# Performance work log

Measured on AMD Instinct MI355X. Metric: run time of the kernel, lower is better.

Reference implementation:

```python
import jax, jax.numpy as jnp
import numpy as np

HEAD_DIM = 256
L2_EPS = 1e-12  # tf.math.l2_normalize default epsilon


def setup_inputs() -> dict:
    key = jax.random.key(0)
    ks = jax.random.split(key, 6)
    B, U = 64, 2048
    D_dec, D_enc = 1024, 512
    H, K, A = 4, HEAD_DIM, 1024
    s = 0.075  # RandomUniform(-0.075, 0.075) kernel init
    return {
        "dec_state": jax.random.normal(ks[0], (B, D_dec), jnp.float32),
        "enc_state": jax.random.normal(ks[1], (B, U, D_enc), jnp.float32),
        "phi_w": jax.random.uniform(ks[2], (H, D_dec, K), jnp.float32, -s, s),
        "phi_b": jnp.zeros((H, K), jnp.float32),
        "psi_w": jax.random.uniform(ks[3], (H, D_enc, K), jnp.float32, -s, s),
        "psi_b": jnp.zeros((H, K), jnp.float32),
        "out_w": jax.random.uniform(ks[4], (H * D_enc, A), jnp.float32, -s, s),
        "out_b": jnp.zeros((A,), jnp.float32),
    }


def reference(dec_state, enc_state, phi_w, phi_b, psi_w, psi_b, out_w, out_b):
    B = dec_state.shape[0]
    # Per-head query/key projections, all heads at once.
    phi_s = jnp.einsum("bd,hdk->bhk", dec_state, phi_w) + phi_b[None]      # (B,H,K)
    psi_h = jnp.einsum("bue,hek->bhuk", enc_state, psi_w) + psi_b[None, :, None]  # (B,H,U,K)
    scale = 1.0 / jnp.sqrt(jnp.asarray(HEAD_DIM, jnp.float32))
    energy = jnp.einsum("bhk,bhuk->bhu", phi_s, psi_h) * scale              # (B,H,U)
    attn = jax.nn.softmax(energy, axis=-1)
    # NOTE: the original attends over the RAW enc_state (not psi_h).
    ctx = jnp.einsum("bhu,bue->bhe", attn, enc_state)                        # (B,H,E)
    # tf.math.l2_normalize over last axis
    sq = jnp.sum(ctx * ctx, axis=-1, keepdims=True)
    ctx = ctx * jax.lax.rsqrt(jnp.maximum(sq, L2_EPS))
    combined = ctx.reshape(B, -1)                                            # (B, H*E) == concat over heads
    return combined @ out_w + out_b
```

## Files before the change

kernel.cpp:

```cpp
#include <hip/hip_runtime.h>
#include <math.h>

typedef float f2 __attribute__((ext_vector_type(2)));

constexpr int NB = 64;
constexpr int NU = 2048;
constexpr int ND = 1024;
constexpr int NE = 512;
constexpr int NH = 4;
constexpr int NK = 256;
constexpr int NA = 1024;
constexpr int NS = 16;
constexpr int ROWS_PER_BLOCK = NU / NS;
constexpr int ROWS_PER_WAVE  = ROWS_PER_BLOCK / 4;
constexpr float SCALE = 0.0625f;

constexpr int RSPLIT = 16;
constexpr int RCH = (NH*NE)/RSPLIT;
constexpr int BT = 8;

constexpr int DSP = 16;

constexpr size_t WS_Q   = 0;
constexpr size_t WS_CTX = WS_Q + (size_t)NB*NH*NE;
constexpr size_t WS_P   = WS_CTX + (size_t)NB*NH*NE;

__global__ __launch_bounds__(256) void k_phi(
    const float* __restrict__ dec, const float* __restrict__ phi_w,
    float* __restrict__ P, float* __restrict__ q, float* __restrict__ ctxacc,
    const float* __restrict__ out_b, float* __restrict__ out)
{
  const int flat = blockIdx.x;
  const int kc = flat & 3;
  const int h  = (flat >> 2) & 3;
  const int ds = flat >> 4;
  const int t = threadIdx.x;

  ctxacc[(size_t)flat*512 + t]       = 0.f;
  ctxacc[(size_t)flat*512 + 256 + t] = 0.f;
  q[(size_t)flat*512 + t]            = 0.f;
  q[(size_t)flat*512 + 256 + t]      = 0.f;
  out[(size_t)flat*256 + t] = out_b[(flat*256 + t) & (NA-1)];

  const int d0 = ds*64, k0 = kc*64;

  __shared__ float phi_lds[64][64];
  __shared__ float dec_t[64][68];

  {
    const int kq = t & 15, r = t >> 4;
    const float* pwb = phi_w + ((size_t)h*ND + d0)*NK + k0;
    #pragma unroll
    for (int p = 0; p < 4; ++p) {
      float4 v = *(const float4*)(pwb + (size_t)(r + 16*p)*NK + 4*kq);
      *(float4*)&phi_lds[r + 16*p][4*kq] = v;
    }
    const float* db = dec + d0 + 4*kq;
    #pragma unroll
    for (int p = 0; p < 4; ++p) {
      const int b = r + 16*p;
      float4 v = *(const float4*)(db + (size_t)b*ND);
      dec_t[4*kq+0][b] = v.x; dec_t[4*kq+1][b] = v.y;
      dec_t[4*kq+2][b] = v.z; dec_t[4*kq+3][b] = v.w;
    }
  }
  __syncthreads();

  const int k = t & 63, bq = t >> 6, b0 = bq*16;
  f2 acc2[8];
  #pragma unroll
  for (int i = 0; i < 8; ++i) acc2[i] = f2{0.f, 0.f};
  #pragma unroll 4
  for (int d = 0; d < 64; ++d) {
    float w = phi_lds[d][k];
    f2 ww = f2{w, w};
    float4 a0 = *(const float4*)&dec_t[d][b0];
    float4 a1 = *(const float4*)&dec_t[d][b0+4];
    float4 a2 = *(const float4*)&dec_t[d][b0+8];
    float4 a3 = *(const float4*)&dec_t[d][b0+12];
    acc2[0] += f2{a0.x,a0.y}*ww; acc2[1] += f2{a0.z,a0.w}*ww;
    acc2[2] += f2{a1.x,a1.y}*ww; acc2[3] += f2{a1.z,a1.w}*ww;
    acc2[4] += f2{a2.x,a2.y}*ww; acc2[5] += f2{a2.z,a2.w}*ww;
    acc2[6] += f2{a3.x,a3.y}*ww; acc2[7] += f2{a3.z,a3.w}*ww;
  }
  float* pb = P + (((size_t)ds*64 + b0)*NH + h)*NK + k0 + k;
  #pragma unroll
  for (int j = 0; j < 8; ++j) {
    pb[(size_t)(2*j  )*NH*NK] = acc2[j][0];
    pb[(size_t)(2*j+1)*NH*NK] = acc2[j][1];
  }
}

__global__ __launch_bounds__(256) void k_q(
    const float* __restrict__ P, const float* __restrict__ phi_b,
    const float* __restrict__ psi_w, float* __restrict__ q)
{
  const int flat = blockIdx.x;
  const int ks = flat & 3;
  const int ec = (flat >> 2) & 7;
  const int h  = flat >> 5;
  const int t = threadIdx.x;
  const int k0 = ks*64, e0 = ec*64;

  __shared__ float phi_red[64][68];
  __shared__ float psi_lds[64][65];

  {
    const int e = t >> 2, kq4 = t & 3;
    const float* pb = psi_w + ((size_t)h*NE + e0 + e)*NK + k0 + 4*kq4;
    #pragma unroll
    for (int p = 0; p < 4; ++p) {
      float4 v = *(const float4*)(pb + 16*p);
      const int kk = 4*(kq4 + 4*p);
      psi_lds[e][kk+0] = v.x; psi_lds[e][kk+1] = v.y;
      psi_lds[e][kk+2] = v.z; psi_lds[e][kk+3] = v.w;
    }
  }
  {
    const int b = t >> 2, kq4 = t & 3;
    const float* pbase = P + ((size_t)b*NH + h)*NK + k0 + 4*kq4;
    #pragma unroll
    for (int p = 0; p < 4; ++p) {
      float4 s = make_float4(0.f, 0.f, 0.f, 0.f);
      #pragma unroll
      for (int dsi = 0; dsi < DSP; ++dsi) {
        float4 v = *(const float4*)(pbase + (size_t)dsi*64*NH*NK + 16*p);
        s.x += v.x; s.y += v.y; s.z += v.z; s.w += v.w;
      }
      const int kk = 4*(kq4 + 4*p);
      const float* bb = phi_b + h*NK + k0 + kk;
      phi_red[kk+0][b] = s.x + bb[0];
      phi_red[kk+1][b] = s.y + bb[1];
      phi_red[kk+2][b] = s.z + bb[2];
      phi_red[kk+3][b] = s.w + bb[3];
    }
  }
  __syncthreads();

  const int e = t & 63, bq = t >> 6, b0 = bq*16;
  f2 acc2[8];
  #pragma unroll
  for (int i = 0; i < 8; ++i) acc2[i] = f2{0.f, 0.f};
  #pragma unroll 4
  for (int kl = 0; kl < 64; ++kl) {
    float w = psi_lds[e][kl];
    f2 ww = f2{w, w};
    float4 a0 = *(const float4*)&phi_red[kl][b0];
    float4 a1 = *(const float4*)&phi_red[kl][b0+4];
    float4 a2 = *(const float4*)&phi_red[kl][b0+8];
    float4 a3 = *(const float4*)&phi_red[kl][b0+12];
    acc2[0] += f2{a0.x,a0.y}*ww; acc2[1] += f2{a0.z,a0.w}*ww;
    acc2[2] += f2{a1.x,a1.y}*ww; acc2[3] += f2{a1.z,a1.w}*ww;
    acc2[4] += f2{a2.x,a2.y}*ww; acc2[5] += f2{a2.z,a2.w}*ww;
    acc2[6] += f2{a3.x,a3.y}*ww; acc2[7] += f2{a3.z,a3.w}*ww;
  }
  float* qb = q + ((size_t)b0*NH + h)*NE + e0 + e;
  #pragma unroll
  for (int j = 0; j < 8; ++j) {
    unsafeAtomicAdd(qb + (size_t)(2*j  )*NH*NE, acc2[j][0]);
    unsafeAtomicAdd(qb + (size_t)(2*j+1)*NH*NE, acc2[j][1]);
  }
}

__global__ __launch_bounds__(256, 4) void k_flash(
    const float* __restrict__ enc, const float* __restrict__ qg,
    float* __restrict__ ctxacc)
{
  const int s = blockIdx.x;
  const int b = blockIdx.y;
  const int t = threadIdx.x;
  const int wave = t >> 6;
  const int lane = t & 63;

  f2 qv[NH][4];
  const float* qb = qg + (size_t)b*NH*NE;
  #pragma unroll
  for (int h = 0; h < NH; ++h) {
    float4 a0 = *(const float4*)(qb + h*NE + 4*lane);
    float4 a1 = *(const float4*)(qb + h*NE + 256 + 4*lane);
    qv[h][0] = f2{a0.x, a0.y}; qv[h][1] = f2{a0.z, a0.w};
    qv[h][2] = f2{a1.x, a1.y}; qv[h][3] = f2{a1.z, a1.w};
  }
  f2 acc2[NH][4];
  #pragma unroll
  for (int h = 0; h < NH; ++h)
    #pragma unroll
    for (int j = 0; j < 4; ++j) acc2[h][j] = f2{0.f, 0.f};

  const int u0 = s*ROWS_PER_BLOCK + wave*ROWS_PER_WAVE;
  const float* encb = enc + ((size_t)b*NU + u0)*NE;
  #pragma unroll 2
  for (int r = 0; r < ROWS_PER_WAVE; ++r) {
    float4 v0 = *(const float4*)(encb + (size_t)r*NE + 4*lane);
    float4 v1 = *(const float4*)(encb + (size_t)r*NE + 256 + 4*lane);
    f2 e0 = f2{v0.x, v0.y}, e1 = f2{v0.z, v0.w};
    f2 e2 = f2{v1.x, v1.y}, e3 = f2{v1.z, v1.w};
    float d[NH];
    #pragma unroll
    for (int h = 0; h < NH; ++h) {
      f2 p = e0*qv[h][0] + e1*qv[h][1] + e2*qv[h][2] + e3*qv[h][3];
      d[h] = p[0] + p[1];
    }
    #pragma unroll
    for (int off = 1; off < 64; off <<= 1) {
      #pragma unroll
      for (int h = 0; h < NH; ++h) d[h] += __shfl_xor(d[h], off);
    }
    #pragma unroll
    for (int h = 0; h < NH; ++h) {
      float pf = __expf(d[h] * SCALE);
      f2 pp = f2{pf, pf};
      acc2[h][0] += pp*e0; acc2[h][1] += pp*e1;
      acc2[h][2] += pp*e2; acc2[h][3] += pp*e3;
    }
  }
  __shared__ float acc_lds[4][NH][NE];
  #pragma unroll
  for (int h = 0; h < NH; ++h) {
    *(float4*)&acc_lds[wave][h][4*lane] =
        make_float4(acc2[h][0][0], acc2[h][0][1], acc2[h][1][0], acc2[h][1][1]);
    *(float4*)&acc_lds[wave][h][256 + 4*lane] =
        make_float4(acc2[h][2][0], acc2[h][2][1], acc2[h][3][0], acc2[h][3][1]);
  }
  __syncthreads();
  float* cb = ctxacc + (size_t)b*(NH*NE);
  #pragma unroll
  for (int h = 0; h < NH; ++h) {
    #pragma unroll
    for (int eo = 0; eo < 2; ++eo) {
      int e = t + eo*256;
      float v = acc_lds[0][h][e] + acc_lds[1][h][e] + acc_lds[2][h][e] + acc_lds[3][h][e];
      unsafeAtomicAdd(&cb[h*NE + e], v);
    }
  }
}

__global__ __launch_bounds__(256) void k_out(
    const float* __restrict__ ctxacc, const float* __restrict__ out_w,
    float* __restrict__ out)
{
  const int t = threadIdx.x;
  const int a = blockIdx.x*256 + t;
  const int b0 = blockIdx.y * BT;
  const int rc = blockIdx.z;
  const int h  = rc >> 2;
  const int e0 = (rc & 3) * RCH;

  __shared__ float rn_lds[BT];
  const int wv = t >> 6, lane = t & 63;
  {
    const int i = 2*wv + (lane >> 5);
    const int l32 = lane & 31;
    const float* row = ctxacc + (size_t)(b0+i)*(NH*NE) + (size_t)h*NE;
    float ss = 0.f;
    #pragma unroll
    for (int j = 0; j < 16; ++j) { float v = row[l32 + 32*j]; ss += v*v; }
    #pragma unroll
    for (int off = 1; off < 32; off <<= 1) ss += __shfl_xor(ss, off);
    if (l32 == 0) rn_lds[i] = rsqrtf(fmaxf(ss, 1e-12f));
  }
  __syncthreads();

  __shared__ float c_lds[RCH][BT];
  for (int g = t; g < RCH*BT; g += 256) {
    const int r = g & (RCH-1), i = g >> 7;
    c_lds[r][i] = ctxacc[(size_t)(b0+i)*(NH*NE) + (size_t)h*NE + e0 + r] * rn_lds[i];
  }
  __syncthreads();

  float accv[BT];
  #pragma unroll
  for (int i = 0; i < BT; ++i) accv[i] = 0.f;
  const float* w = out_w + ((size_t)rc*RCH)*NA + a;
  #pragma unroll 8
  for (int r = 0; r < RCH; ++r) {
    float wvv = w[(size_t)r*NA];
    float4 ca = *(const float4*)&c_lds[r][0];
    float4 cb = *(const float4*)&c_lds[r][4];
    accv[0] += ca.x*wvv; accv[1] += ca.y*wvv; accv[2] += ca.z*wvv; accv[3] += ca.w*wvv;
    accv[4] += cb.x*wvv; accv[5] += cb.y*wvv; accv[6] += cb.z*wvv; accv[7] += cb.w*wvv;
  }
  #pragma unroll
  for (int i = 0; i < BT; ++i)
    unsafeAtomicAdd(&out[(size_t)(b0+i)*NA + a], accv[i]);
}

extern "C" void kernel_launch(void* const* d_in, const int* in_sizes, int n_in,
                              void* d_out, int out_size, void* d_ws, size_t ws_size,
                              hipStream_t stream) {
  const float* dec   = (const float*)d_in[0];
  const float* enc   = (const float*)d_in[1];
  const float* phi_w = (const float*)d_in[2];
  const float* phi_b = (const float*)d_in[3];
  const float* psi_w = (const float*)d_in[4];
  const float* out_w = (const float*)d_in[6];
  const float* out_b = (const float*)d_in[7];
  float* out = (float*)d_out;
  float* ws = (float*)d_ws;
  float* q      = ws + WS_Q;
  float* ctxacc = ws + WS_CTX;
  float* P      = ws + WS_P;

  hipLaunchKernelGGL(k_phi,   dim3(NH*4*DSP),              dim3(256), 0, stream,
                     dec, phi_w, P, q, ctxacc, out_b, out);
  hipLaunchKernelGGL(k_q,     dim3(128),                   dim3(256), 0, stream,
                     P, phi_b, psi_w, q);
  hipLaunchKernelGGL(k_flash, dim3(NS, NB),                dim3(256), 0, stream,
                     enc, q, ctxacc);
  hipLaunchKernelGGL(k_out,   dim3(NA/256, NB/BT, RSPLIT), dim3(256), 0, stream,
                     ctxacc, out_w, out);
}
```

Measured before the change: 84.71 us.

## Double-buffer encoder rows into LDS with async global_load_lds in flash kernel

The flash kernel now streams encoder rows through a per-wave double-buffered LDS staging area using direct global-to-LDS loads. It waits on vmcnt so the next two rows are in flight while the current two are processed, which is meant to hide global memory latency. It also folds the softmax scale into q up front, drops the occupancy hint in launch_bounds, and reuses the staging buffer for the final reduction. The risks are LDS round-trip overhead, reliance on manual waitcnt correctness, and possibly lower occupancy.

After: 91.18 us. +7.6%, slower.

```diff
diff --git a/kernel.cpp b/kernel.cpp
--- a/kernel.cpp
+++ b/kernel.cpp
@@ -162,7 +162,7 @@
   }
 }
 
-__global__ __launch_bounds__(256, 4) void k_flash(
+__global__ __launch_bounds__(256) void k_flash(
     const float* __restrict__ enc, const float* __restrict__ qg,
     float* __restrict__ ctxacc)
 {
@@ -172,14 +172,16 @@
   const int wave = t >> 6;
   const int lane = t & 63;
 
+  __shared__ float sbuf[4][2][2*NE];
+
   f2 qv[NH][4];
   const float* qb = qg + (size_t)b*NH*NE;
   #pragma unroll
   for (int h = 0; h < NH; ++h) {
     float4 a0 = *(const float4*)(qb + h*NE + 4*lane);
     float4 a1 = *(const float4*)(qb + h*NE + 256 + 4*lane);
-    qv[h][0] = f2{a0.x, a0.y}; qv[h][1] = f2{a0.z, a0.w};
-    qv[h][2] = f2{a1.x, a1.y}; qv[h][3] = f2{a1.z, a1.w};
+    qv[h][0] = f2{a0.x*SCALE, a0.y*SCALE}; qv[h][1] = f2{a0.z*SCALE, a0.w*SCALE};
+    qv[h][2] = f2{a1.x*SCALE, a1.y*SCALE}; qv[h][3] = f2{a1.z*SCALE, a1.w*SCALE};
   }
   f2 acc2[NH][4];
   #pragma unroll
@@ -189,37 +191,65 @@
 
   const int u0 = s*ROWS_PER_BLOCK + wave*ROWS_PER_WAVE;
   const float* encb = enc + ((size_t)b*NU + u0)*NE;
-  #pragma unroll 2
-  for (int r = 0; r < ROWS_PER_WAVE; ++r) {
-    float4 v0 = *(const float4*)(encb + (size_t)r*NE + 4*lane);
-    float4 v1 = *(const float4*)(encb + (size_t)r*NE + 256 + 4*lane);
-    f2 e0 = f2{v0.x, v0.y}, e1 = f2{v0.z, v0.w};
-    f2 e2 = f2{v1.x, v1.y}, e3 = f2{v1.z, v1.w};
-    float d[NH];
-    #pragma unroll
-    for (int h = 0; h < NH; ++h) {
-      f2 p = e0*qv[h][0] + e1*qv[h][1] + e2*qv[h][2] + e3*qv[h][3];
-      d[h] = p[0] + p[1];
-    }
-    #pragma unroll
-    for (int off = 1; off < 64; off <<= 1) {
+
+  auto STAGE = [&](int c, int buf) {
+    const float* src = encb + (size_t)c*2*NE + 4*lane;
+    float* dst = &sbuf[wave][buf][0];
+    #pragma unroll
+    for (int i = 0; i < 4; ++i) {
+      __builtin_amdgcn_global_load_lds(
+          (const __attribute__((address_space(1))) void*)(src + i*256),
+          (__attribute__((address_space(3))) void*)(dst + i*256),
+          16, 0, 0);
+    }
+  };
+
+  STAGE(0, 0);
+  int cur = 0;
+  for (int c = 0; c < ROWS_PER_WAVE/2; ++c) {
+    if (c < ROWS_PER_WAVE/2 - 1) {
+      STAGE(c+1, cur^1);
+      asm volatile("s_waitcnt vmcnt(4)" ::: "memory");
+    } else {
+      asm volatile("s_waitcnt vmcnt(0)" ::: "memory");
+    }
+    __builtin_amdgcn_sched_barrier(0);
+    const float* rowbase = &sbuf[wave][cur][0];
+    #pragma unroll
+    for (int rr = 0; rr < 2; ++rr) {
+      float4 v0 = *(const float4*)(rowbase + rr*NE + 4*lane);
+      float4 v1 = *(const float4*)(rowbase + rr*NE + 256 + 4*lane);
+      f2 e0 = f2{v0.x, v0.y}, e1 = f2{v0.z, v0.w};
+      f2 e2 = f2{v1.x, v1.y}, e3 = f2{v1.z, v1.w};
+      float d[NH];
       #pragma unroll
-      for (int h = 0; h < NH; ++h) d[h] += __shfl_xor(d[h], off);
-    }
-    #pragma unroll
-    for (int h = 0; h < NH; ++h) {
-      float pf = __expf(d[h] * SCALE);
-      f2 pp = f2{pf, pf};
-      acc2[h][0] += pp*e0; acc2[h][1] += pp*e1;
-      acc2[h][2] += pp*e2; acc2[h][3] += pp*e3;
-    }
-  }
-  __shared__ float acc_lds[4][NH][NE];
+      for (int h = 0; h < NH; ++h) {
+        f2 p = e0*qv[h][0] + e1*qv[h][1] + e2*qv[h][2] + e3*qv[h][3];
+        d[h] = p[0] + p[1];
+      }
+      #pragma unroll
+      for (int off = 1; off < 64; off <<= 1) {
+        #pragma unroll
+        for (int h = 0; h < NH; ++h) d[h] += __shfl_xor(d[h], off);
+      }
+      #pragma unroll
+      for (int h = 0; h < NH; ++h) {
+        float pf = __expf(d[h]);
+        f2 pp = f2{pf, pf};
+        acc2[h][0] += pp*e0; acc2[h][1] += pp*e1;
+        acc2[h][2] += pp*e2; acc2[h][3] += pp*e3;
+      }
+    }
+    cur ^= 1;
+  }
+
+  __syncthreads();
+  float* acc_lds = &sbuf[0][0][0];
   #pragma unroll
   for (int h = 0; h < NH; ++h) {
-    *(float4*)&acc_lds[wave][h][4*lane] =
+    *(float4*)&acc_lds[(wave*NH + h)*NE + 4*lane] =
         make_float4(acc2[h][0][0], acc2[h][0][1], acc2[h][1][0], acc2[h][1][1]);
-    *(float4*)&acc_lds[wave][h][256 + 4*lane] =
+    *(float4*)&acc_lds[(wave*NH + h)*NE + 256 + 4*lane] =
         make_float4(acc2[h][2][0], acc2[h][2][1], acc2[h][3][0], acc2[h][3][1]);
   }
   __syncthreads();
@@ -229,7 +259,8 @@
     #pragma unroll
     for (int eo = 0; eo < 2; ++eo) {
       int e = t + eo*256;
-      float v = acc_lds[0][h][e] + acc_lds[1][h][e] + acc_lds[2][h][e] + acc_lds[3][h][e];
+      float v = acc_lds[(0*NH + h)*NE + e] + acc_lds[(1*NH + h)*NE + e]
+              + acc_lds[(2*NH + h)*NE + e] + acc_lds[(3*NH + h)*NE + e];
       unsafeAtomicAdd(&cb[h*NE + e], v);
     }
   }
```

## Process two encoder rows per wave with half-wave split and software-prefetched loads

Applied to the files above, without the earlier changes.

The flash kernel now has each half-wave (32 lanes) handle one encoder row, so a wave covers two rows per step. The dot-product reduction shrinks from six to five shuffle stages, and the shuffles are packed in pairs of heads. Loads are double-buffered by hand so the next row pair is fetched while the current one is computed, and SCALE is folded into q once up front. The cost is twice as many q and accumulator registers per lane, and the occupancy hint in launch_bounds is dropped, which may lower waves per CU.

New measurement: 80.67 us. -4.8%, faster.

```diff
diff --git a/kernel.cpp b/kernel.cpp
--- a/kernel.cpp
+++ b/kernel.cpp
@@ -162,7 +162,11 @@
   }
 }
 
-__global__ __launch_bounds__(256, 4) void k_flash(
+__device__ __forceinline__ f2 shflx(f2 v, int m) {
+  return f2{__shfl_xor(v[0], m), __shfl_xor(v[1], m)};
+}
+
+__global__ __launch_bounds__(256) void k_flash(
     const float* __restrict__ enc, const float* __restrict__ qg,
     float* __restrict__ ctxacc)
 {
@@ -171,56 +175,103 @@
   const int t = threadIdx.x;
   const int wave = t >> 6;
   const int lane = t & 63;
-
-  f2 qv[NH][4];
-  const float* qb = qg + (size_t)b*NH*NE;
-  #pragma unroll
-  for (int h = 0; h < NH; ++h) {
-    float4 a0 = *(const float4*)(qb + h*NE + 4*lane);
-    float4 a1 = *(const float4*)(qb + h*NE + 256 + 4*lane);
-    qv[h][0] = f2{a0.x, a0.y}; qv[h][1] = f2{a0.z, a0.w};
-    qv[h][2] = f2{a1.x, a1.y}; qv[h][3] = f2{a1.z, a1.w};
-  }
-  f2 acc2[NH][4];
+  const int half = lane >> 5;
+  const int l32 = lane & 31;
+
+  f2 qv[NH][8];
+  const float* qbase = qg + (size_t)b*NH*NE + 4*l32;
   #pragma unroll
   for (int h = 0; h < NH; ++h)
     #pragma unroll
-    for (int j = 0; j < 4; ++j) acc2[h][j] = f2{0.f, 0.f};
+    for (int ch = 0; ch < 4; ++ch) {
+      float4 a = *(const float4*)(qbase + h*NE + ch*128);
+      qv[h][2*ch]   = f2{a.x*SCALE, a.y*SCALE};
+      qv[h][2*ch+1] = f2{a.z*SCALE, a.w*SCALE};
+    }
+
+  f2 acc2[NH][8];
+  #pragma unroll
+  for (int h = 0; h < NH; ++h)
+    #pragma unroll
+    for (int j = 0; j < 8; ++j) acc2[h][j] = f2{0.f, 0.f};
 
   const int u0 = s*ROWS_PER_BLOCK + wave*ROWS_PER_WAVE;
-  const float* encb = enc + ((size_t)b*NU + u0)*NE;
+  const float* myrow = enc + ((size_t)b*NU + u0 + half)*NE + 4*l32;
+
+#define FLOAD(d0_, d1_, d2_, d3_, it) { \
+    const float* rp_ = myrow + (size_t)(it)*2*NE; \
+    d0_ = *(const float4*)(rp_);       d1_ = *(const float4*)(rp_ + 128); \
+    d2_ = *(const float4*)(rp_ + 256); d3_ = *(const float4*)(rp_ + 384); }
+
+#define FCOMP(x0, x1, x2, x3) { \
+    f2 p0 = f2{x0.x,x0.y}*qv[0][0] + f2{x0.z,x0.w}*qv[0][1] \
+          + f2{x1.x,x1.y}*qv[0][2] + f2{x1.z,x1.w}*qv[0][3] \
+          + f2{x2.x,x2.y}*qv[0][4] + f2{x2.z,x2.w}*qv[0][5] \
+          + f2{x3.x,x3.y}*qv[0][6] + f2{x3.z,x3.w}*qv[0][7]; \
+    f2 p1 = f2{x0.x,x0.y}*qv[1][0] + f2{x0.z,x0.w}*qv[1][1] \
+          + f2{x1.x,x1.y}*qv[1][2] + f2{x1.z,x1.w}*qv[1][3] \
+          + f2{x2.x,x2.y}*qv[1][4] + f2{x2.z,x2.w}*qv[1][5] \
+          + f2{x3.x,x3.y}*qv[1][6] + f2{x3.z,x3.w}*qv[1][7]; \
+    f2 p2 = f2{x0.x,x0.y}*qv[2][0] + f2{x0.z,x0.w}*qv[2][1] \
+          + f2{x1.x,x1.y}*qv[2][2] + f2{x1.z,x1.w}*qv[2][3] \
+          + f2{x2.x,x2.y}*qv[2][4] + f2{x2.z,x2.w}*qv[2][5] \
+          + f2{x3.x,x3.y}*qv[2][6] + f2{x3.z,x3.w}*qv[2][7]; \
+    f2 p3 = f2{x0.x,x0.y}*qv[3][0] + f2{x0.z,x0.w}*qv[3][1] \
+          + f2{x1.x,x1.y}*qv[3][2] + f2{x1.z,x1.w}*qv[3][3] \
+          + f2{x2.x,x2.y}*qv[3][4] + f2{x2.z,x2.w}*qv[3][5] \
+          + f2{x3.x,x3.y}*qv[3][6] + f2{x3.z,x3.w}*qv[3][7]; \
+    f2 d01 = f2{p0[0]+p0[1], p1[0]+p1[1]}; \
+    f2 d23 = f2{p2[0]+p2[1], p3[0]+p3[1]}; \
+    d01 += shflx(d01, 1);  d23 += shflx(d23, 1); \
+    d01 += shflx(d01, 2);  d23 += shflx(d23, 2); \
+    d01 += shflx(d01, 4);  d23 += shflx(d23, 4); \
+    d01 += shflx(d01, 8);  d23 += shflx(d23, 8); \
+    d01 += shflx(d01, 16); d23 += shflx(d23, 16); \
+    float w0 = __expf(d01[0]), w1 = __expf(d01[1]); \
+    float w2 = __expf(d23[0]), w3 = __expf(d23[1]); \
+    acc2[0][0]+=f2{w0,w0}*f2{x0.x,x0.y}; acc2[0][1]+=f2{w0,w0}*f2{x0.z,x0.w}; \
+    acc2[0][2]+=f2{w0,w0}*f2{x1.x,x1.y}; acc2[0][3]+=f2{w0,w0}*f2{x1.z,x1.w}; \
+    acc2[0][4]+=f2{w0,w0}*f2{x2.x,x2.y}; acc2[0][5]+=f2{w0,w0}*f2{x2.z,x2.w}; \
+    acc2[0][6]+=f2{w0,w0}*f2{x3.x,x3.y}; acc2[0][7]+=f2{w0,w0}*f2{x3.z,x3.w}; \
+    acc2[1][0]+=f2{w1,w1}*f2{x0.x,x0.y}; acc2[1][1]+=f2{w1,w1}*f2{x0.z,x0.w}; \
+    acc2[1][2]+=f2{w1,w1}*f2{x1.x,x1.y}; acc2[1][3]+=f2{w1,w1}*f2{x1.z,x1.w}; \
+    acc2[1][4]+=f2{w1,w1}*f2{x2.x,x2.y}; acc2[1][5]+=f2{w1,w1}*f2{x2.z,x2.w}; \
+    acc2[1][6]+=f2{w1,w1}*f2{x3.x,x3.y}; acc2[1][7]+=f2{w1,w1}*f2{x3.z,x3.w}; \
+    acc2[2][0]+=f2{w2,w2}*f2{x0.x,x0.y}; acc2[2][1]+=f2{w2,w2}*f2{x0.z,x0.w}; \
+    acc2[2][2]+=f2{w2,w2}*f2{x1.x,x1.y}; acc2[2][3]+=f2{w2,w2}*f2{x1.z,x1.w}; \
+    acc2[2][4]+=f2{w2,w2}*f2{x2.x,x2.y}; acc2[2][5]+=f2{w2,w2}*f2{x2.z,x2.w}; \
+    acc2[2][6]+=f2{w2,w2}*f2{x3.x,x3.y}; acc2[2][7]+=f2{w2,w2}*f2{x3.z,x3.w}; \
+    acc2[3][0]+=f2{w3,w3}*f2{x0.x,x0.y}; acc2[3][1]+=f2{w3,w3}*f2{x0.z,x0.w}; \
+    acc2[3][2]+=f2{w3,w3}*f2{x1.x,x1.y}; acc2[3][3]+=f2{w3,w3}*f2{x1.z,x1.w}; \
+    acc2[3][4]+=f2{w3,w3}*f2{x2.x,x2.y}; acc2[3][5]+=f2{w3,w3}*f2{x2.z,x2.w}; \
+    acc2[3][6]+=f2{w3,w3}*f2{x3.x,x3.y}; acc2[3][7]+=f2{w3,w3}*f2{x3.z,x3.w}; }
+
+  float4 A0,A1,A2,A3, B0,B1,B2,B3;
+  FLOAD(A0,A1,A2,A3, 0)
   #pragma unroll 2
-  for (int r = 0; r < ROWS_PER_WAVE; ++r) {
-    float4 v0 = *(const float4*)(encb + (size_t)r*NE + 4*lane);
-    float4 v1 = *(const float4*)(encb + (size_t)r*NE + 256 + 4*lane);
-    f2 e0 = f2{v0.x, v0.y}, e1 = f2{v0.z, v0.w};
-    f2 e2 = f2{v1.x, v1.y}, e3 = f2{v1.z, v1.w};
-    float d[NH];
-    #pragma unroll
-    for (int h = 0; h < NH; ++h) {
-      f2 p = e0*qv[h][0] + e1*qv[h][1] + e2*qv[h][2] + e3*qv[h][3];
-      d[h] = p[0] + p[1];
-    }
-    #pragma unroll
-    for (int off = 1; off < 64; off <<= 1) {
+  for (int i = 0; i < ROWS_PER_WAVE/2; i += 2) {
+    if (i + 1 < ROWS_PER_WAVE/2) FLOAD(B0,B1,B2,B3, i+1)
+    FCOMP(A0,A1,A2,A3)
+    if (i + 2 < ROWS_PER_WAVE/2) FLOAD(A0,A1,A2,A3, i+2)
+    if (i + 1 < ROWS_PER_WAVE/2) FCOMP(B0,B1,B2,B3)
+  }
+#undef FLOAD
+#undef FCOMP
+
+  #pragma unroll
+  for (int h = 0; h < NH; ++h)
+    #pragma unroll
+    for (int j = 0; j < 8; ++j) acc2[h][j] += shflx(acc2[h][j], 32);
+
+  __shared__ float acc_lds[4*NH*NE];
+  if (half == 0) {
+    #pragma unroll
+    for (int h = 0; h < NH; ++h)
       #pragma unroll
-      for (int h = 0; h < NH; ++h) d[h] += __shfl_xor(d[h], off);
-    }
-    #pragma unroll
-    for (int h = 0; h < NH; ++h) {
-      float pf = __expf(d[h] * SCALE);
-      f2 pp = f2{pf, pf};
-      acc2[h][0] += pp*e0; acc2[h][1] += pp*e1;
-      acc2[h][2] += pp*e2; acc2[h][3] += pp*e3;
-    }
-  }
-  __shared__ float acc_lds[4][NH][NE];
-  #pragma unroll
-  for (int h = 0; h < NH; ++h) {
-    *(float4*)&acc_lds[wave][h][4*lane] =
-        make_float4(acc2[h][0][0], acc2[h][0][1], acc2[h][1][0], acc2[h][1][1]);
-    *(float4*)&acc_lds[wave][h][256 + 4*lane] =
-        make_float4(acc2[h][2][0], acc2[h][2][1], acc2[h][3][0], acc2[h][3][1]);
+      for (int ch = 0; ch < 4; ++ch)
+        *(float4*)&acc_lds[(wave*NH + h)*NE + ch*128 + 4*l32] =
+            make_float4(acc2[h][2*ch][0], acc2[h][2*ch][1],
+                        acc2[h][2*ch+1][0], acc2[h][2*ch+1][1]);
   }
   __syncthreads();
   float* cb = ctxacc + (size_t)b*(NH*NE);
@@ -229,7 +280,8 @@
     #pragma unroll
     for (int eo = 0; eo < 2; ++eo) {
       int e = t + eo*256;
-      float v = acc_lds[0][h][e] + acc_lds[1][h][e] + acc_lds[2][h][e] + acc_lds[3][h][e];
+      float v = acc_lds[(0*NH + h)*NE + e] + acc_lds[(1*NH + h)*NE + e]
+              + acc_lds[(2*NH + h)*NE + e] + acc_lds[(3*NH + h)*NE + e];
       unsafeAtomicAdd(&cb[h*NE + e], v);
     }
   }
```

## Split waves into half-wave row pairs with 4-deep register prefetch in flash kernel

Applied to the files above, without the earlier changes.

Each wave now processes two encoder rows at once, one per 32-lane half, so the dot-product reduction needs five shuffle steps instead of six and covers two rows per step. Encoder rows are prefetched into a 4-slot register ring so loads for later iterations are in flight while the current row is computed. The softmax scale is folded into q at load time, and the two halves are merged with a final xor-32 shuffle. The cost is many more registers, since q and the accumulators double per thread and there are 16 float4 prefetch slots, and the occupancy hint was removed from launch bounds.

Measured after the change: 79.90 us. -5.7%, faster.

```diff
diff --git a/kernel.cpp b/kernel.cpp
--- a/kernel.cpp
+++ b/kernel.cpp
@@ -162,7 +162,50 @@
   }
 }
 
-__global__ __launch_bounds__(256, 4) void k_flash(
+__device__ __forceinline__ f2 shflx(f2 v, int m) {
+  return f2{__shfl_xor(v[0], m), __shfl_xor(v[1], m)};
+}
+
+__device__ __forceinline__ void fload(float4 (&r)[4], const float* myrow, int it) {
+  const float* rp = myrow + (size_t)it*2*NE;
+  r[0] = *(const float4*)(rp);
+  r[1] = *(const float4*)(rp + 128);
+  r[2] = *(const float4*)(rp + 256);
+  r[3] = *(const float4*)(rp + 384);
+}
+
+__device__ __forceinline__ void fcomp(const float4 (&x)[4],
+                                      const f2 (&qv)[NH][8], f2 (&acc2)[NH][8]) {
+  f2 xf[8];
+  xf[0]=f2{x[0].x,x[0].y}; xf[1]=f2{x[0].z,x[0].w};
+  xf[2]=f2{x[1].x,x[1].y}; xf[3]=f2{x[1].z,x[1].w};
+  xf[4]=f2{x[2].x,x[2].y}; xf[5]=f2{x[2].z,x[2].w};
+  xf[6]=f2{x[3].x,x[3].y}; xf[7]=f2{x[3].z,x[3].w};
+  f2 p[NH];
+  #pragma unroll
+  for (int h = 0; h < NH; ++h) {
+    p[h] = xf[0]*qv[h][0];
+    #pragma unroll
+    for (int j = 1; j < 8; ++j) p[h] += xf[j]*qv[h][j];
+  }
+  f2 d01 = f2{p[0][0]+p[0][1], p[1][0]+p[1][1]};
+  f2 d23 = f2{p[2][0]+p[2][1], p[3][0]+p[3][1]};
+  #pragma unroll
+  for (int off = 1; off < 32; off <<= 1) {
+    d01 += shflx(d01, off);
+    d23 += shflx(d23, off);
+  }
+  const float w[NH] = {__expf(d01[0]), __expf(d01[1]),
+                       __expf(d23[0]), __expf(d23[1])};
+  #pragma unroll
+  for (int h = 0; h < NH; ++h) {
+    f2 ww = f2{w[h], w[h]};
+    #pragma unroll
+    for (int j = 0; j < 8; ++j) acc2[h][j] += ww*xf[j];
+  }
+}
+
+__global__ __launch_bounds__(256) void k_flash(
     const float* __restrict__ enc, const float* __restrict__ qg,
     float* __restrict__ ctxacc)
 {
@@ -171,56 +214,53 @@
   const int t = threadIdx.x;
   const int wave = t >> 6;
   const int lane = t & 63;
-
-  f2 qv[NH][4];
-  const float* qb = qg + (size_t)b*NH*NE;
-  #pragma unroll
-  for (int h = 0; h < NH; ++h) {
-    float4 a0 = *(const float4*)(qb + h*NE + 4*lane);
-    float4 a1 = *(const float4*)(qb + h*NE + 256 + 4*lane);
-    qv[h][0] = f2{a0.x, a0.y}; qv[h][1] = f2{a0.z, a0.w};
-    qv[h][2] = f2{a1.x, a1.y}; qv[h][3] = f2{a1.z, a1.w};
-  }
-  f2 acc2[NH][4];
+  const int half = lane >> 5;
+  const int l32 = lane & 31;
+
+  f2 qv[NH][8];
+  const float* qbase = qg + (size_t)b*NH*NE + 4*l32;
   #pragma unroll
   for (int h = 0; h < NH; ++h)
     #pragma unroll
-    for (int j = 0; j < 4; ++j) acc2[h][j] = f2{0.f, 0.f};
+    for (int ch = 0; ch < 4; ++ch) {
+      float4 a = *(const float4*)(qbase + h*NE + ch*128);
+      qv[h][2*ch]   = f2{a.x*SCALE, a.y*SCALE};
+      qv[h][2*ch+1] = f2{a.z*SCALE, a.w*SCALE};
+    }
+
+  f2 acc2[NH][8];
+  #pragma unroll
+  for (int h = 0; h < NH; ++h)
+    #pragma unroll
+    for (int j = 0; j < 8; ++j) acc2[h][j] = f2{0.f, 0.f};
 
   const int u0 = s*ROWS_PER_BLOCK + wave*ROWS_PER_WAVE;
-  const float* encb = enc + ((size_t)b*NU + u0)*NE;
-  #pragma unroll 2
-  for (int r = 0; r < ROWS_PER_WAVE; ++r) {
-    float4 v0 = *(const float4*)(encb + (size_t)r*NE + 4*lane);
-    float4 v1 = *(const float4*)(encb + (size_t)r*NE + 256 + 4*lane);
-    f2 e0 = f2{v0.x, v0.y}, e1 = f2{v0.z, v0.w};
-    f2 e2 = f2{v1.x, v1.y}, e3 = f2{v1.z, v1.w};
-    float d[NH];
-    #pragma unroll
-    for (int h = 0; h < NH; ++h) {
-      f2 p = e0*qv[h][0] + e1*qv[h][1] + e2*qv[h][2] + e3*qv[h][3];
-      d[h] = p[0] + p[1];
-    }
-    #pragma unroll
-    for (int off = 1; off < 64; off <<= 1) {
+  const float* myrow = enc + ((size_t)b*NU + u0 + half)*NE + 4*l32;
+
+  constexpr int NIT = ROWS_PER_WAVE/2;
+  float4 R[4][4];
+  #pragma unroll
+  for (int c = 0; c < 4; ++c) fload(R[c], myrow, c);
+  #pragma unroll
+  for (int i = 0; i < NIT; ++i) {
+    fcomp(R[i & 3], qv, acc2);
+    if (i + 4 < NIT) fload(R[i & 3], myrow, i + 4);
+  }
+
+  #pragma unroll
+  for (int h = 0; h < NH; ++h)
+    #pragma unroll
+    for (int j = 0; j < 8; ++j) acc2[h][j] += shflx(acc2[h][j], 32);
+
+  __shared__ float acc_lds[4*NH*NE];
+  if (half == 0) {
+    #pragma unroll
+    for (int h = 0; h < NH; ++h)
       #pragma unroll
-      for (int h = 0; h < NH; ++h) d[h] += __shfl_xor(d[h], off);
-    }
-    #pragma unroll
-    for (int h = 0; h < NH; ++h) {
-      float pf = __expf(d[h] * SCALE);
-      f2 pp = f2{pf, pf};
-      acc2[h][0] += pp*e0; acc2[h][1] += pp*e1;
-      acc2[h][2] += pp*e2; acc2[h][3] += pp*e3;
-    }
-  }
-  __shared__ float acc_lds[4][NH][NE];
-  #pragma unroll
-  for (int h = 0; h < NH; ++h) {
-    *(float4*)&acc_lds[wave][h][4*lane] =
-        make_float4(acc2[h][0][0], acc2[h][0][1], acc2[h][1][0], acc2[h][1][1]);
-    *(float4*)&acc_lds[wave][h][256 + 4*lane] =
-        make_float4(acc2[h][2][0], acc2[h][2][1], acc2[h][3][0], acc2[h][3][1]);
+      for (int ch = 0; ch < 4; ++ch)
+        *(float4*)&acc_lds[(wave*NH + h)*NE + ch*128 + 4*l32] =
+            make_float4(acc2[h][2*ch][0], acc2[h][2*ch][1],
+                        acc2[h][2*ch+1][0], acc2[h][2*ch+1][1]);
   }
   __syncthreads();
   float* cb = ctxacc + (size_t)b*(NH*NE);
@@ -229,7 +269,8 @@
     #pragma unroll
     for (int eo = 0; eo < 2; ++eo) {
       int e = t + eo*256;
-      float v = acc_lds[0][h][e] + acc_lds[1][h][e] + acc_lds[2][h][e] + acc_lds[3][h][e];
+      float v = acc_lds[(0*NH + h)*NE + e] + acc_lds[(1*NH + h)*NE + e]
+              + acc_lds[(2*NH + h)*NE + e] + acc_lds[(3*NH + h)*NE + e];
       unsafeAtomicAdd(&cb[h*NE + e], v);
     }
   }
```
